# Kernel tuning notes

Hardware: AMD Instinct MI355X
Metric: run time of the kernel (lower is better)

## Reference

```python
import jax, jax.numpy as jnp
import numpy as np

N_USERS = 16384
EMB_DIM = 32
N_EDGES = 524288  # N_USERS * avg_degree 32


def setup_inputs() -> dict:
    key = jax.random.key(0)
    k1, k2, k3, k4, k5 = jax.random.split(key, 5)
    social_emb = jax.random.normal(k1, (N_USERS, EMB_DIM), dtype=jnp.float32)
    preference_emb = jax.random.normal(k2, (N_USERS, EMB_DIM), dtype=jnp.float32)
    # Jaccard similarities lie in [0, 1]
    attention_scores = jax.random.uniform(k3, (N_USERS, N_USERS), dtype=jnp.float32)
    uu_graph = jax.random.randint(k4, (2, N_EDGES), 0, N_USERS, dtype=jnp.int64)
    return {
        "social_emb": social_emb,
        "preference_emb": preference_emb,
        "attention_scores": attention_scores,
        "uu_graph": uu_graph,
    }


def reference(social_emb, preference_emb, attention_scores, uu_graph):
    # The original per-user Python loop:
    #   final[i] = sum_j attention_scores[i, j] * preference_emb[j]
    # is exactly one dense [N,N] @ [N,D] matmul.
    final = attention_scores @ preference_emb  # [N, D]
    # prop_uu: one round of message passing over the user-user graph
    # (sum of source-user embeddings into each destination user).
    src, dst = uu_graph[0], uu_graph[1]
    out = jax.ops.segment_sum(final[src], dst, num_segments=final.shape[0])  # [N, D]
    # dropout is identity at inference (rate treated as 0)
    return out
```

## Files before the change

### kernel.cpp

```cpp
#include <hip/hip_runtime.h>
#include <hip/hip_bf16.h>

#define NUSERS 16384
#define DIM 32
#define NEDGES 524288
#define KCHUNK 32
#define KTILE 256
#define NTILES (NUSERS / KTILE)
#define RPB 64
#define CAP 192
#define NGEMM (NUSERS / RPB)
#define NBUCK 256

using f32x4  = __attribute__((ext_vector_type(4))) float;
using bf16x8 = __attribute__((ext_vector_type(8))) short;
using s16x4  = __attribute__((ext_vector_type(4))) short;
using int4v  = __attribute__((ext_vector_type(4))) int;
using int2v  = __attribute__((ext_vector_type(2))) int;

static __device__ __forceinline__ short f2bf(float f) {
    __hip_bfloat16 h = __float2bfloat16(f);
    return __builtin_bit_cast(short, h);
}

static __device__ __forceinline__ bool detect_is64(const int* __restrict__ g) {
    bool is64 = true;
#pragma unroll
    for (int s = 0; s < 8; ++s) is64 &= (g[2 * s + 1] == 0);
    return is64;
}

__global__ void __launch_bounds__(256) prep_pfrag(const float* __restrict__ P,
                                                  short* __restrict__ Pfrag,
                                                  int* __restrict__ cursor) {
    int t = blockIdx.x * blockDim.x + threadIdx.x;
    if (t < NUSERS) cursor[t] = 0;
    int lane = t & 63;
    int h    = (t >> 6) & 1;
    int c    = t >> 7;
    int d    = h * 16 + (lane & 15);
    int gq   = lane >> 4;
    short tmp[8];
#pragma unroll
    for (int i = 0; i < 8; ++i)
        tmp[i] = f2bf(P[(size_t)(c * KCHUNK + gq * 8 + i) * DIM + d]);
    *reinterpret_cast<bf16x8*>(Pfrag + (size_t)t * 8) =
        *reinterpret_cast<bf16x8*>(tmp);
}

__global__ void __launch_bounds__(256, 2) gemm_bucket(const float* __restrict__ A,
                                                      const short* __restrict__ Pfrag,
                                                      float* __restrict__ fin,
                                                      const int* __restrict__ g,
                                                      int* __restrict__ cursor,
                                                      int* __restrict__ bucket) {
    __shared__ short lds[4][2][16][256];

    if (blockIdx.x >= NGEMM) {
        bool is64 = detect_is64(g);
        int base = (blockIdx.x - NGEMM) * (NEDGES / NBUCK);
#pragma unroll
        for (int k = 0; k < NEDGES / NBUCK / 256; ++k) {
            int e = base + k * 256 + threadIdx.x;
            int src, dst;
            if (is64) {
                const int2v* g2 = reinterpret_cast<const int2v*>(g);
                src = g2[e].x;
                dst = g2[NEDGES + e].x;
            } else {
                src = g[e];
                dst = g[NEDGES + e];
            }
            int p = atomicAdd(&cursor[dst], 1);
            if (p < CAP) bucket[(size_t)dst * CAP + p] = src;
        }
        return;
    }

    const int lane = threadIdx.x & 63;
    const int wave = threadIdx.x >> 6;
    const int r    = lane & 15;
    const int gq   = lane >> 4;

    const int row0 = blockIdx.x * RPB + wave * 16;
    const float* Abase = A + (size_t)row0 * NUSERS;

    short* buf0 = &lds[wave][0][0][0];
    short* buf1 = &lds[wave][1][0][0];

    f32x4  acc0 = {0.f, 0.f, 0.f, 0.f};
    f32x4  acc1 = {0.f, 0.f, 0.f, 0.f};
    f32x4  sreg[16];
    bf16x8 bregA[16], bregB[16];

    auto issueA = [&](int t) {
#pragma unroll
        for (int k = 0; k < 16; ++k)
            sreg[k] = *reinterpret_cast<const f32x4*>(
                Abase + (size_t)k * NUSERS + t * KTILE + lane * 4);
    };
    auto issueB = [&](int t, bf16x8* br) {
        const short* pf = Pfrag + (size_t)t * 8192;
#pragma unroll
        for (int cc = 0; cc < 8; ++cc) {
            br[2 * cc]     = *reinterpret_cast<const bf16x8*>(pf + cc * 1024 + lane * 8);
            br[2 * cc + 1] = *reinterpret_cast<const bf16x8*>(pf + cc * 1024 + 512 + lane * 8);
        }
    };
    auto commitT = [&](short* buf) {
#pragma unroll
        for (int k = 0; k < 16; ++k) {
            int cb = (lane * 8) ^ ((k & 7) << 4);
            s16x4 v = {f2bf(sreg[k][0]), f2bf(sreg[k][1]),
                       f2bf(sreg[k][2]), f2bf(sreg[k][3])};
            *reinterpret_cast<s16x4*>(buf + k * 256 + (cb >> 1)) = v;
        }
        asm volatile("s_waitcnt lgkmcnt(0)" ::: "memory");
        __builtin_amdgcn_sched_barrier(0);
    };
    auto computeT = [&](const bf16x8* br, const short* buf) {
#pragma unroll
        for (int cc = 0; cc < 8; ++cc) {
            int cb = (cc * 64 + gq * 16) ^ ((r & 7) << 4);
            bf16x8 af = *reinterpret_cast<const bf16x8*>(buf + r * 256 + (cb >> 1));
            acc0 = __builtin_amdgcn_mfma_f32_16x16x32_bf16(af, br[2 * cc],     acc0, 0, 0, 0);
            acc1 = __builtin_amdgcn_mfma_f32_16x16x32_bf16(af, br[2 * cc + 1], acc1, 0, 0, 0);
        }
    };

    issueA(0);
    issueB(0, bregA);
    commitT(buf0);

    for (int t = 0; t < NTILES; t += 2) {
        issueA(t + 1);
        issueB(t + 1, bregB);
        computeT(bregA, buf0);
        commitT(buf1);
        if (t + 2 < NTILES) {
            issueA(t + 2);
            issueB(t + 2, bregA);
        }
        computeT(bregB, buf1);
        if (t + 2 < NTILES) commitT(buf0);
    }

    const int out_row0 = row0 + gq * 4;
#pragma unroll
    for (int q = 0; q < 4; ++q) {
        float* dst = fin + (size_t)(out_row0 + q) * DIM + r;
        dst[0]  = acc0[q];
        dst[16] = acc1[q];
    }
}

__global__ void __launch_bounds__(256) gather_kernel(const int* __restrict__ bucket,
                                                     const int* __restrict__ cursor,
                                                     const float* __restrict__ fin,
                                                     float* __restrict__ out) {
    int t = blockIdx.x * blockDim.x + threadIdx.x;
    int d = t >> 3;
    int q = t & 7;
    if (d >= NUSERS) return;
    int cnt = cursor[d];
    if (cnt > CAP) cnt = CAP;
    const int* bk = bucket + (size_t)d * CAP;
    const f32x4* f4 = reinterpret_cast<const f32x4*>(fin);
    f32x4 s = {0.f, 0.f, 0.f, 0.f};
    int i = 0;
    for (; i + 4 <= cnt; i += 4) {
        int4v s4 = *reinterpret_cast<const int4v*>(bk + i);
        s += f4[(size_t)s4.x * 8 + q];
        s += f4[(size_t)s4.y * 8 + q];
        s += f4[(size_t)s4.z * 8 + q];
        s += f4[(size_t)s4.w * 8 + q];
    }
    for (; i < cnt; ++i)
        s += f4[(size_t)bk[i] * 8 + q];
    reinterpret_cast<f32x4*>(out)[(size_t)d * 8 + q] = s;
}

extern "C" void kernel_launch(void* const* d_in, const int* in_sizes, int n_in,
                              void* d_out, int out_size, void* d_ws, size_t ws_size,
                              hipStream_t stream) {
    const float* pref = (const float*)d_in[1];
    const float* att  = (const float*)d_in[2];
    const int*   grph = (const int*)d_in[3];
    float* out = (float*)d_out;

    char* ws = (char*)d_ws;
    float* fin    = (float*)ws;
    short* pfrag  = (short*)(ws + (size_t)18 * 1024 * 1024);
    int*   cursor = (int*)  (ws + (size_t)19 * 1024 * 1024);
    int*   bucket = (int*)  (ws + (size_t)20 * 1024 * 1024);

    prep_pfrag<<<dim3(256), dim3(256), 0, stream>>>(pref, pfrag, cursor);

    gemm_bucket<<<dim3(NGEMM + NBUCK), dim3(256), 0, stream>>>(
        att, pfrag, fin, grph, cursor, bucket);

    gather_kernel<<<dim3(NUSERS * 8 / 256), dim3(256), 0, stream>>>(bucket, cursor, fin, out);
}
```

Before: 211.4 us.

## Split GEMM K dimension in two and fold edge bucketing into every block

The dense GEMM now splits the K dimension into two halves, giving 512 blocks (256 row blocks × 2 K-segments) instead of 256. Each block writes a partial result, and a new reduce kernel sums the two partials. The edge-bucketing work, which used to run in separate extra blocks, is now spread across all GEMM blocks at the start. This aims to fill more CUs on the GPU and balance load, at the cost of an extra kernel launch and a partial-buffer round trip through memory.

```diff
diff --git a/kernel.cpp b/kernel.cpp
--- a/kernel.cpp
+++ b/kernel.cpp
@@ -6,11 +6,12 @@
 #define NEDGES 524288
 #define KCHUNK 32
 #define KTILE 256
-#define NTILES (NUSERS / KTILE)
+#define KSPLIT 2
+#define KHALF (NUSERS / KSPLIT)
+#define NTILES_K (KHALF / KTILE)
 #define RPB 64
 #define CAP 192
-#define NGEMM (NUSERS / RPB)
-#define NBUCK 256
+#define NGEMM 512
 
 using f32x4  = __attribute__((ext_vector_type(4))) float;
 using bf16x8 = __attribute__((ext_vector_type(8))) short;
@@ -48,19 +49,19 @@
         *reinterpret_cast<bf16x8*>(tmp);
 }
 
-__global__ void __launch_bounds__(256, 2) gemm_bucket(const float* __restrict__ A,
-                                                      const short* __restrict__ Pfrag,
-                                                      float* __restrict__ fin,
-                                                      const int* __restrict__ g,
-                                                      int* __restrict__ cursor,
-                                                      int* __restrict__ bucket) {
+__global__ void __launch_bounds__(256, 2) gemm2(const float* __restrict__ A,
+                                                const short* __restrict__ Pfrag,
+                                                float* __restrict__ parts,
+                                                const int* __restrict__ g,
+                                                int* __restrict__ cursor,
+                                                int* __restrict__ bucket) {
     __shared__ short lds[4][2][16][256];
 
-    if (blockIdx.x >= NGEMM) {
+    {
         bool is64 = detect_is64(g);
-        int base = (blockIdx.x - NGEMM) * (NEDGES / NBUCK);
-#pragma unroll
-        for (int k = 0; k < NEDGES / NBUCK / 256; ++k) {
+        int base = blockIdx.x * (NEDGES / NGEMM);
+#pragma unroll
+        for (int k = 0; k < NEDGES / NGEMM / 256; ++k) {
             int e = base + k * 256 + threadIdx.x;
             int src, dst;
             if (is64) {
@@ -74,7 +75,6 @@
             int p = atomicAdd(&cursor[dst], 1);
             if (p < CAP) bucket[(size_t)dst * CAP + p] = src;
         }
-        return;
     }
 
     const int lane = threadIdx.x & 63;
@@ -82,8 +82,11 @@
     const int r    = lane & 15;
     const int gq   = lane >> 4;
 
-    const int row0 = blockIdx.x * RPB + wave * 16;
-    const float* Abase = A + (size_t)row0 * NUSERS;
+    const int rowblk = blockIdx.x & 255;
+    const int kseg   = blockIdx.x >> 8;
+    const int row0   = rowblk * RPB + wave * 16;
+    const float* Abase  = A + (size_t)row0 * NUSERS + (size_t)kseg * KHALF;
+    const short* Pfbase = Pfrag + (size_t)kseg * (KHALF / KCHUNK) * 1024;
 
     short* buf0 = &lds[wave][0][0][0];
     short* buf1 = &lds[wave][1][0][0];
@@ -100,7 +103,7 @@
                 Abase + (size_t)k * NUSERS + t * KTILE + lane * 4);
     };
     auto issueB = [&](int t, bf16x8* br) {
-        const short* pf = Pfrag + (size_t)t * 8192;
+        const short* pf = Pfbase + (size_t)t * 8192;
 #pragma unroll
         for (int cc = 0; cc < 8; ++cc) {
             br[2 * cc]     = *reinterpret_cast<const bf16x8*>(pf + cc * 1024 + lane * 8);
@@ -132,26 +135,35 @@
     issueB(0, bregA);
     commitT(buf0);
 
-    for (int t = 0; t < NTILES; t += 2) {
+    for (int t = 0; t < NTILES_K; t += 2) {
         issueA(t + 1);
         issueB(t + 1, bregB);
         computeT(bregA, buf0);
         commitT(buf1);
-        if (t + 2 < NTILES) {
+        if (t + 2 < NTILES_K) {
             issueA(t + 2);
             issueB(t + 2, bregA);
         }
         computeT(bregB, buf1);
-        if (t + 2 < NTILES) commitT(buf0);
-    }
-
+        if (t + 2 < NTILES_K) commitT(buf0);
+    }
+
+    float* part = parts + (size_t)kseg * NUSERS * DIM;
     const int out_row0 = row0 + gq * 4;
 #pragma unroll
     for (int q = 0; q < 4; ++q) {
-        float* dst = fin + (size_t)(out_row0 + q) * DIM + r;
+        float* dst = part + (size_t)(out_row0 + q) * DIM + r;
         dst[0]  = acc0[q];
         dst[16] = acc1[q];
     }
+}
+
+__global__ void __launch_bounds__(256) reduce2(const float* __restrict__ parts,
+                                               float* __restrict__ fin) {
+    int i = blockIdx.x * blockDim.x + threadIdx.x;
+    const f32x4* p4 = reinterpret_cast<const f32x4*>(parts);
+    reinterpret_cast<f32x4*>(fin)[i] =
+        p4[i] + p4[(size_t)(NUSERS * DIM / 4) + i];
 }
 
 __global__ void __launch_bounds__(256) gather_kernel(const int* __restrict__ bucket,
@@ -193,11 +205,13 @@
     short* pfrag  = (short*)(ws + (size_t)18 * 1024 * 1024);
     int*   cursor = (int*)  (ws + (size_t)19 * 1024 * 1024);
     int*   bucket = (int*)  (ws + (size_t)20 * 1024 * 1024);
+    float* parts  = (float*)(ws + (size_t)32 * 1024 * 1024);
 
     prep_pfrag<<<dim3(256), dim3(256), 0, stream>>>(pref, pfrag, cursor);
 
-    gemm_bucket<<<dim3(NGEMM + NBUCK), dim3(256), 0, stream>>>(
-        att, pfrag, fin, grph, cursor, bucket);
+    gemm2<<<dim3(NGEMM), dim3(256), 0, stream>>>(att, pfrag, parts, grph, cursor, bucket);
+
+    reduce2<<<dim3(NUSERS * DIM / 4 / 256), dim3(256), 0, stream>>>(parts, fin);
 
     gather_kernel<<<dim3(NUSERS * 8 / 256), dim3(256), 0, stream>>>(bucket, cursor, fin, out);
 }
```

Result: slower. 225.7 us (+6.8%).
